# Kernel optimization log

Hardware: AMD Instinct MI355X
Metric: run time of the kernel (lower is better)

The kernel has to match this reference:

```python
import jax, jax.numpy as jnp
import numpy as np

B, N, D = 8, 256, 256
LN_EPS = 1e-5


def setup_inputs() -> dict:
    key = jax.random.key(0)
    ks = jax.random.split(key, 8)
    s1 = 1.0 / np.sqrt(2 * D)  # torch Linear init scale ~ U(-1/sqrt(fan_in), ...); use normal*scale
    s2 = 1.0 / np.sqrt(D)
    return {
        "patch_features": jax.random.normal(ks[0], (B, N, D), dtype=jnp.float32),
        # relation_transform: Linear(2D, D) -> ReLU -> Linear(D, 1)
        "W1": jax.random.normal(ks[1], (2 * D, D), dtype=jnp.float32) * s1,
        "b1": jax.random.normal(ks[2], (D,), dtype=jnp.float32) * s1,
        "W2": jax.random.normal(ks[3], (D, 1), dtype=jnp.float32) * s2,
        "b2": jax.random.normal(ks[4], (1,), dtype=jnp.float32) * s2,
        # context_projection: Linear(D, D) + LayerNorm(D)
        "Wp": jax.random.normal(ks[5], (D, D), dtype=jnp.float32) * s2,
        "bp": jax.random.normal(ks[6], (D,), dtype=jnp.float32) * s2,
        "ln_gamma": jnp.ones((D,), dtype=jnp.float32),
        "ln_beta": jnp.zeros((D,), dtype=jnp.float32),
    }


def reference(patch_features, W1, b1, W2, b2, Wp, bp, ln_gamma, ln_beta):
    x = patch_features  # [B, N, D]
    d = x.shape[-1]
    # cat([x_i, x_j]) @ W1 == x_i @ W1[:D] + x_j @ W1[D:]
    hi = jnp.einsum("bnd,de->bne", x, W1[:d])   # [B, N, D]
    hj = jnp.einsum("bmd,de->bme", x, W1[d:])   # [B, N, D]
    h = jax.nn.relu(hi[:, :, None, :] + hj[:, None, :, :] + b1)  # [B, N, N, D]
    scores = jnp.einsum("bnmd,do->bnm", h, W2) + b2[0]            # [B, N, N]
    # diagonal entries stay exactly 0 (original never fills i == j)
    eye = jnp.eye(scores.shape[1], dtype=bool)
    scores = jnp.where(eye[None, :, :], 0.0, scores)
    weights = jax.nn.softmax(scores, axis=2)                      # [B, N, N]
    ctx = jnp.einsum("bnm,bmd->bnd", weights, x)                  # [B, N, D]
    proj = jnp.einsum("bnd,de->bne", ctx, Wp) + bp
    mu = jnp.mean(proj, axis=-1, keepdims=True)
    var = jnp.mean(jnp.square(proj - mu), axis=-1, keepdims=True)
    ln = (proj - mu) * jax.lax.rsqrt(var + LN_EPS) * ln_gamma + ln_beta
    return x + ln
```

## Files before the change

kernel.cpp:

```cpp
#include <hip/hip_runtime.h>

#define LN_EPS 1e-5f

__device__ __forceinline__ float wred_max(float v) {
#pragma unroll
    for (int off = 32; off; off >>= 1) v = fmaxf(v, __shfl_xor(v, off, 64));
    return v;
}
__device__ __forceinline__ float wred_sum(float v) {
#pragma unroll
    for (int off = 32; off; off >>= 1) v += __shfl_xor(v, off, 64);
    return v;
}


#define GL(Q, KB) { const float* _p = Wb + (size_t)((KB) * 8) * 256;            \
    _Pragma("unroll") for (int _j = 0; _j < 8; _j++)                            \
        Q[_j] = *(const float2*)(_p + (size_t)_j * 256); }

#define GC(Q, KB) { const int _k = (KB) * 8;                                    \
    _Pragma("unroll") for (int _r = 0; _r < 4; _r++) {                          \
        float4 _xa = *(const float4*)(xr + _r * 256 + _k);                      \
        float4 _xb = *(const float4*)(xr + _r * 256 + _k + 4);                  \
        acc[_r][0] = fmaf(_xa.x, Q[0].x, acc[_r][0]);                           \
        acc[_r][1] = fmaf(_xa.x, Q[0].y, acc[_r][1]);                           \
        acc[_r][0] = fmaf(_xa.y, Q[1].x, acc[_r][0]);                           \
        acc[_r][1] = fmaf(_xa.y, Q[1].y, acc[_r][1]);                           \
        acc[_r][0] = fmaf(_xa.z, Q[2].x, acc[_r][0]);                           \
        acc[_r][1] = fmaf(_xa.z, Q[2].y, acc[_r][1]);                           \
        acc[_r][0] = fmaf(_xa.w, Q[3].x, acc[_r][0]);                           \
        acc[_r][1] = fmaf(_xa.w, Q[3].y, acc[_r][1]);                           \
        acc[_r][0] = fmaf(_xb.x, Q[4].x, acc[_r][0]);                           \
        acc[_r][1] = fmaf(_xb.x, Q[4].y, acc[_r][1]);                           \
        acc[_r][0] = fmaf(_xb.y, Q[5].x, acc[_r][0]);                           \
        acc[_r][1] = fmaf(_xb.y, Q[5].y, acc[_r][1]);                           \
        acc[_r][0] = fmaf(_xb.z, Q[6].x, acc[_r][0]);                           \
        acc[_r][1] = fmaf(_xb.z, Q[6].y, acc[_r][1]);                           \
        acc[_r][0] = fmaf(_xb.w, Q[7].x, acc[_r][0]);                           \
        acc[_r][1] = fmaf(_xb.w, Q[7].y, acc[_r][1]); } }

__global__ __launch_bounds__(256) void k_gemm_hij(
    const float* __restrict__ x,
    const float* __restrict__ W1,
    const float* __restrict__ b1,
    float* __restrict__ hi_ws,
    float* __restrict__ hjT)
{
    __shared__ __align__(16) float xs[8][256];
    const int t = threadIdx.x;
    const int lane = t & 63, w = t >> 6;
    const int b = blockIdx.x & 7;
    const int idx = blockIdx.x >> 3;
    const int rg = idx & 31;
    const int half = idx >> 5;
    const int mrow0 = rg * 8;

    {
        const float4* src = (const float4*)(x + (size_t)(b * 256 + mrow0) * 256);
        ((float4*)xs)[t]       = src[t];
        ((float4*)xs)[t + 256] = src[t + 256];
    }
    __syncthreads();

    const int rsub = (w >> 1) * 4;
    const int e0 = ((w & 1) << 7) + 2 * lane;
    const float* Wb = W1 + (size_t)half * 65536 + e0;
    const float* xr = &xs[rsub][0];

    float acc[4][2];
#pragma unroll
    for (int r = 0; r < 4; r++) { acc[r][0] = 0.f; acc[r][1] = 0.f; }

    float2 qa[8], qb[8];
    GL(qa, 0);
    for (int kb = 0; kb + 2 < 32; kb += 2) {
        GL(qb, kb + 1);
        GC(qa, kb);
        GL(qa, kb + 2);
        GC(qb, kb + 1);
    }
    GL(qb, 31);
    GC(qa, 30);
    GC(qb, 31);

    if (half == 0) {
        const int grow0 = b * 256 + mrow0 + rsub;
        float2 bb = *(const float2*)(b1 + e0);
#pragma unroll
        for (int r = 0; r < 4; r++)
            *(float2*)&hi_ws[(size_t)(grow0 + r) * 256 + e0] =
                make_float2(acc[r][0] + bb.x, acc[r][1] + bb.y);
    } else {
        const int m0 = mrow0 + rsub;
        *(float4*)&hjT[(size_t)b * 65536 + (size_t)e0 * 256 + m0] =
            make_float4(acc[0][0], acc[1][0], acc[2][0], acc[3][0]);
        *(float4*)&hjT[(size_t)b * 65536 + (size_t)(e0 + 1) * 256 + m0] =
            make_float4(acc[0][1], acc[1][1], acc[2][1], acc[3][1]);
    }
}


#define P1L(H, G) { const float* _p = hjp + (size_t)((G) * 4) * 256;            \
    _Pragma("unroll") for (int _j = 0; _j < 4; _j++)                            \
        H[_j] = *(const float4*)(_p + (size_t)_j * 256); }

#define P1C(H, G) { const int _db = w * 64 + (G) * 4;                           \
    float4 _wq = *(const float4*)&w2_s[_db];                                    \
    _Pragma("unroll") for (int _n = 0; _n < 4; _n++) {                          \
        float4 _h4 = *(const float4*)&hi_s[_n][_db];                            \
        sp[_n][0] = fmaf(fmaxf(_h4.x + H[0].x, 0.f), _wq.x, sp[_n][0]);         \
        sp[_n][0] = fmaf(fmaxf(_h4.y + H[1].x, 0.f), _wq.y, sp[_n][0]);         \
        sp[_n][0] = fmaf(fmaxf(_h4.z + H[2].x, 0.f), _wq.z, sp[_n][0]);         \
        sp[_n][0] = fmaf(fmaxf(_h4.w + H[3].x, 0.f), _wq.w, sp[_n][0]);         \
        sp[_n][1] = fmaf(fmaxf(_h4.x + H[0].y, 0.f), _wq.x, sp[_n][1]);         \
        sp[_n][1] = fmaf(fmaxf(_h4.y + H[1].y, 0.f), _wq.y, sp[_n][1]);         \
        sp[_n][1] = fmaf(fmaxf(_h4.z + H[2].y, 0.f), _wq.z, sp[_n][1]);         \
        sp[_n][1] = fmaf(fmaxf(_h4.w + H[3].y, 0.f), _wq.w, sp[_n][1]);         \
        sp[_n][2] = fmaf(fmaxf(_h4.x + H[0].z, 0.f), _wq.x, sp[_n][2]);         \
        sp[_n][2] = fmaf(fmaxf(_h4.y + H[1].z, 0.f), _wq.y, sp[_n][2]);         \
        sp[_n][2] = fmaf(fmaxf(_h4.z + H[2].z, 0.f), _wq.z, sp[_n][2]);         \
        sp[_n][2] = fmaf(fmaxf(_h4.w + H[3].z, 0.f), _wq.w, sp[_n][2]);         \
        sp[_n][3] = fmaf(fmaxf(_h4.x + H[0].w, 0.f), _wq.x, sp[_n][3]);         \
        sp[_n][3] = fmaf(fmaxf(_h4.y + H[1].w, 0.f), _wq.y, sp[_n][3]);         \
        sp[_n][3] = fmaf(fmaxf(_h4.z + H[2].w, 0.f), _wq.z, sp[_n][3]);         \
        sp[_n][3] = fmaf(fmaxf(_h4.w + H[3].w, 0.f), _wq.w, sp[_n][3]); } }

#define DLOAD(X, PTR, G) { const float* _p = (PTR) + (size_t)((G) * 8) * 256;   \
    _Pragma("unroll") for (int _j = 0; _j < 8; _j++)                            \
        X[_j] = *(const float4*)(_p + (size_t)_j * 256); }

#define DCOMP(ACCV, WS, X, G) { const int _rb = w * 64 + (G) * 8;               \
    _Pragma("unroll") for (int _n = 0; _n < 4; _n++) {                          \
        float4 _wa = *(const float4*)&WS[_n][_rb];                              \
        float4 _wb = *(const float4*)&WS[_n][_rb + 4];                          \
        ACCV[_n][0] = fmaf(_wa.x, X[0].x, ACCV[_n][0]);                         \
        ACCV[_n][0] = fmaf(_wa.y, X[1].x, ACCV[_n][0]);                         \
        ACCV[_n][0] = fmaf(_wa.z, X[2].x, ACCV[_n][0]);                         \
        ACCV[_n][0] = fmaf(_wa.w, X[3].x, ACCV[_n][0]);                         \
        ACCV[_n][0] = fmaf(_wb.x, X[4].x, ACCV[_n][0]);                         \
        ACCV[_n][0] = fmaf(_wb.y, X[5].x, ACCV[_n][0]);                         \
        ACCV[_n][0] = fmaf(_wb.z, X[6].x, ACCV[_n][0]);                         \
        ACCV[_n][0] = fmaf(_wb.w, X[7].x, ACCV[_n][0]);                         \
        ACCV[_n][1] = fmaf(_wa.x, X[0].y, ACCV[_n][1]);                         \
        ACCV[_n][1] = fmaf(_wa.y, X[1].y, ACCV[_n][1]);                         \
        ACCV[_n][1] = fmaf(_wa.z, X[2].y, ACCV[_n][1]);                         \
        ACCV[_n][1] = fmaf(_wa.w, X[3].y, ACCV[_n][1]);                         \
        ACCV[_n][1] = fmaf(_wb.x, X[4].y, ACCV[_n][1]);                         \
        ACCV[_n][1] = fmaf(_wb.y, X[5].y, ACCV[_n][1]);                         \
        ACCV[_n][1] = fmaf(_wb.z, X[6].y, ACCV[_n][1]);                         \
        ACCV[_n][1] = fmaf(_wb.w, X[7].y, ACCV[_n][1]);                         \
        ACCV[_n][2] = fmaf(_wa.x, X[0].z, ACCV[_n][2]);                         \
        ACCV[_n][2] = fmaf(_wa.y, X[1].z, ACCV[_n][2]);                         \
        ACCV[_n][2] = fmaf(_wa.z, X[2].z, ACCV[_n][2]);                         \
        ACCV[_n][2] = fmaf(_wa.w, X[3].z, ACCV[_n][2]);                         \
        ACCV[_n][2] = fmaf(_wb.x, X[4].z, ACCV[_n][2]);                         \
        ACCV[_n][2] = fmaf(_wb.y, X[5].z, ACCV[_n][2]);                         \
        ACCV[_n][2] = fmaf(_wb.z, X[6].z, ACCV[_n][2]);                         \
        ACCV[_n][2] = fmaf(_wb.w, X[7].z, ACCV[_n][2]);                         \
        ACCV[_n][3] = fmaf(_wa.x, X[0].w, ACCV[_n][3]);                         \
        ACCV[_n][3] = fmaf(_wa.y, X[1].w, ACCV[_n][3]);                         \
        ACCV[_n][3] = fmaf(_wa.z, X[2].w, ACCV[_n][3]);                         \
        ACCV[_n][3] = fmaf(_wa.w, X[3].w, ACCV[_n][3]);                         \
        ACCV[_n][3] = fmaf(_wb.x, X[4].w, ACCV[_n][3]);                         \
        ACCV[_n][3] = fmaf(_wb.y, X[5].w, ACCV[_n][3]);                         \
        ACCV[_n][3] = fmaf(_wb.z, X[6].w, ACCV[_n][3]);                         \
        ACCV[_n][3] = fmaf(_wb.w, X[7].w, ACCV[_n][3]); } }

__global__ __launch_bounds__(256) void k_fused(
    const float* __restrict__ x,
    const float* __restrict__ hi_ws,
    const float* __restrict__ hjT,
    const float* __restrict__ W2, const float* __restrict__ b2,
    const float* __restrict__ Wp, const float* __restrict__ bp,
    const float* __restrict__ gma, const float* __restrict__ bta,
    float* __restrict__ out)
{
    const int t = threadIdx.x;
    const int lane = t & 63, w = t >> 6;
    const int b = blockIdx.x & 7;
    const int n0 = (blockIdx.x >> 3) * 4;
    const int bn0 = b * 256 + n0;

    __shared__ __align__(16) float hi_s[4][256];
    __shared__ __align__(16) float w2_s[256];
    __shared__ __align__(16) float wt_s[4][256];
    __shared__ __align__(16) float ctx_s[4][256];
    __shared__ __align__(16) float sred[4][4][256];
    __shared__ float part[8][4];

#pragma unroll
    for (int i = 0; i < 4; i++) hi_s[i][t] = hi_ws[(size_t)(bn0 + i) * 256 + t];
    w2_s[t] = W2[t];
    __syncthreads();

    {
        const float* hjp = hjT + (size_t)b * 65536 + (size_t)(w * 64) * 256 + 4 * lane;
        float sp[4][4];
#pragma unroll
        for (int n = 0; n < 4; n++)
#pragma unroll
            for (int j = 0; j < 4; j++) sp[n][j] = 0.f;

        float4 ha[4], hb[4];
        P1L(ha, 0);
        for (int g = 0; g + 2 < 16; g += 2) {
            P1L(hb, g + 1);
            P1C(ha, g);
            P1L(ha, g + 2);
            P1C(hb, g + 1);
        }
        P1L(hb, 15);
        P1C(ha, 14);
        P1C(hb, 15);

#pragma unroll
        for (int n = 0; n < 4; n++)
            *(float4*)&sred[w][n][4 * lane] =
                make_float4(sp[n][0], sp[n][1], sp[n][2], sp[n][3]);
    }
    __syncthreads();

    float b2v = b2[0];
    float s[4];
#pragma unroll
    for (int i = 0; i < 4; i++) {
        s[i] = ((sred[0][i][t] + sred[1][i][t]) +
                (sred[2][i][t] + sred[3][i][t])) + b2v;
        if (t == n0 + i) s[i] = 0.f;
    }
#pragma unroll
    for (int i = 0; i < 4; i++) {
        float m = wred_max(s[i]);
        if (lane == 0) part[i][w] = m;
    }
    __syncthreads();
    float ev[4];
#pragma unroll
    for (int i = 0; i < 4; i++) {
        float mx = fmaxf(fmaxf(part[i][0], part[i][1]),
                         fmaxf(part[i][2], part[i][3]));
        ev[i] = __expf(s[i] - mx);
        float sm = wred_sum(ev[i]);
        if (lane == 0) part[4 + i][w] = sm;
    }
    __syncthreads();
#pragma unroll
    for (int i = 0; i < 4; i++) {
        float tot = (part[4 + i][0] + part[4 + i][1]) +
                    (part[4 + i][2] + part[4 + i][3]);
        wt_s[i][t] = ev[i] / tot;
    }
    __syncthreads();

    {
        const float* xpp = x + (size_t)b * 65536 + (size_t)(w * 64) * 256 + 4 * lane;
        float cp[4][4];
#pragma unroll
        for (int n = 0; n < 4; n++)
#pragma unroll
            for (int j = 0; j < 4; j++) cp[n][j] = 0.f;

        float4 xa[8], xb[8];
        DLOAD(xa, xpp, 0);
        for (int g = 0; g + 2 < 8; g += 2) {
            DLOAD(xb, xpp, g + 1);
            DCOMP(cp, wt_s, xa, g);
            DLOAD(xa, xpp, g + 2);
            DCOMP(cp, wt_s, xb, g + 1);
        }
        DLOAD(xb, xpp, 7);
        DCOMP(cp, wt_s, xa, 6);
        DCOMP(cp, wt_s, xb, 7);

#pragma unroll
        for (int n = 0; n < 4; n++)
            *(float4*)&sred[w][n][4 * lane] =
                make_float4(cp[n][0], cp[n][1], cp[n][2], cp[n][3]);
    }
    __syncthreads();
#pragma unroll
    for (int i = 0; i < 4; i++)
        ctx_s[i][t] = (sred[0][i][t] + sred[1][i][t]) +
                      (sred[2][i][t] + sred[3][i][t]);
    __syncthreads();

    {
        const float* wpp = Wp + (size_t)(w * 64) * 256 + 4 * lane;
        float pq[4][4];
#pragma unroll
        for (int n = 0; n < 4; n++)
#pragma unroll
            for (int j = 0; j < 4; j++) pq[n][j] = 0.f;

        float4 qa4[8], qb4[8];
        DLOAD(qa4, wpp, 0);
        for (int g = 0; g + 2 < 8; g += 2) {
            DLOAD(qb4, wpp, g + 1);
            DCOMP(pq, ctx_s, qa4, g);
            DLOAD(qa4, wpp, g + 2);
            DCOMP(pq, ctx_s, qb4, g + 1);
        }
        DLOAD(qb4, wpp, 7);
        DCOMP(pq, ctx_s, qa4, 6);
        DCOMP(pq, ctx_s, qb4, 7);

#pragma unroll
        for (int n = 0; n < 4; n++)
            *(float4*)&sred[w][n][4 * lane] =
                make_float4(pq[n][0], pq[n][1], pq[n][2], pq[n][3]);
    }
    __syncthreads();

    float bpv = bp[t];
    float p[4];
#pragma unroll
    for (int i = 0; i < 4; i++)
        p[i] = ((sred[0][i][t] + sred[1][i][t]) +
                (sred[2][i][t] + sred[3][i][t])) + bpv;

#pragma unroll
    for (int i = 0; i < 4; i++) {
        float su = wred_sum(p[i]);
        float sq = wred_sum(p[i] * p[i]);
        if (lane == 0) { part[i][w] = su; part[4 + i][w] = sq; }
    }
    __syncthreads();
    float gv = gma[t], bv = bta[t];
#pragma unroll
    for (int i = 0; i < 4; i++) {
        float su = (part[i][0] + part[i][1]) + (part[i][2] + part[i][3]);
        float sq = (part[4 + i][0] + part[4 + i][1]) +
                   (part[4 + i][2] + part[4 + i][3]);
        float mu = su * (1.f / 256.f);
        float var = sq * (1.f / 256.f) - mu * mu;
        float ln = (p[i] - mu) * rsqrtf(var + LN_EPS) * gv + bv;
        out[(size_t)(bn0 + i) * 256 + t] = x[(size_t)(bn0 + i) * 256 + t] + ln;
    }
}

extern "C" void kernel_launch(void* const* d_in, const int* in_sizes, int n_in,
                              void* d_out, int out_size, void* d_ws, size_t ws_size,
                              hipStream_t stream) {
    const float* x   = (const float*)d_in[0];
    const float* W1  = (const float*)d_in[1];
    const float* b1  = (const float*)d_in[2];
    const float* W2  = (const float*)d_in[3];
    const float* b2  = (const float*)d_in[4];
    const float* Wp  = (const float*)d_in[5];
    const float* bp  = (const float*)d_in[6];
    const float* gma = (const float*)d_in[7];
    const float* bta = (const float*)d_in[8];
    float* out = (float*)d_out;

    float* hi_ws = (float*)d_ws;
    float* hjT   = hi_ws + (size_t)2048 * 256;

    k_gemm_hij<<<512, 256, 0, stream>>>(x, W1, b1, hi_ws, hjT);
    k_fused<<<512, 256, 0, stream>>>(x, hi_ws, hjT, W2, b2, Wp, bp,
                                     gma, bta, out);
}
```

Measured before the change: 107.8 us.

## Remap hi/hj GEMM threads to one row by eight columns with float4 weight loads

Changes the thread mapping of the first projection GEMM so each thread computes one row and eight output columns, in place of four rows and two columns. Weights are now loaded as float4 rather than float2, and the shared-memory tile is padded to 260 columns to avoid bank conflicts. Launch bounds now request two blocks per SM. In exchange, each weight element is reused across only one row instead of four, which raises global and L2 weight traffic, and the transposed hj stores become scalar strided writes instead of float4.

Result: slower. 121.7 us (+12.9%).

```diff
diff --git a/kernel.cpp b/kernel.cpp
--- a/kernel.cpp
+++ b/kernel.cpp
@@ -14,39 +14,33 @@
 }
 
 
-#define GL(Q, KB) { const float* _p = Wb + (size_t)((KB) * 8) * 256;            \
-    _Pragma("unroll") for (int _j = 0; _j < 8; _j++)                            \
-        Q[_j] = *(const float2*)(_p + (size_t)_j * 256); }
-
-#define GC(Q, KB) { const int _k = (KB) * 8;                                    \
-    _Pragma("unroll") for (int _r = 0; _r < 4; _r++) {                          \
-        float4 _xa = *(const float4*)(xr + _r * 256 + _k);                      \
-        float4 _xb = *(const float4*)(xr + _r * 256 + _k + 4);                  \
-        acc[_r][0] = fmaf(_xa.x, Q[0].x, acc[_r][0]);                           \
-        acc[_r][1] = fmaf(_xa.x, Q[0].y, acc[_r][1]);                           \
-        acc[_r][0] = fmaf(_xa.y, Q[1].x, acc[_r][0]);                           \
-        acc[_r][1] = fmaf(_xa.y, Q[1].y, acc[_r][1]);                           \
-        acc[_r][0] = fmaf(_xa.z, Q[2].x, acc[_r][0]);                           \
-        acc[_r][1] = fmaf(_xa.z, Q[2].y, acc[_r][1]);                           \
-        acc[_r][0] = fmaf(_xa.w, Q[3].x, acc[_r][0]);                           \
-        acc[_r][1] = fmaf(_xa.w, Q[3].y, acc[_r][1]);                           \
-        acc[_r][0] = fmaf(_xb.x, Q[4].x, acc[_r][0]);                           \
-        acc[_r][1] = fmaf(_xb.x, Q[4].y, acc[_r][1]);                           \
-        acc[_r][0] = fmaf(_xb.y, Q[5].x, acc[_r][0]);                           \
-        acc[_r][1] = fmaf(_xb.y, Q[5].y, acc[_r][1]);                           \
-        acc[_r][0] = fmaf(_xb.z, Q[6].x, acc[_r][0]);                           \
-        acc[_r][1] = fmaf(_xb.z, Q[6].y, acc[_r][1]);                           \
-        acc[_r][0] = fmaf(_xb.w, Q[7].x, acc[_r][0]);                           \
-        acc[_r][1] = fmaf(_xb.w, Q[7].y, acc[_r][1]); } }
-
-__global__ __launch_bounds__(256) void k_gemm_hij(
+#define WL(Q, XQ, C) {                                                          \
+    XQ = *(const float4*)&xs[row_local][(C) * 4];                               \
+    const float* _wp = Wb + (size_t)((C) * 4) * 256;                            \
+    _Pragma("unroll") for (int _j = 0; _j < 4; _j++) {                          \
+        Q[2 * _j]     = *(const float4*)(_wp + (size_t)_j * 256);               \
+        Q[2 * _j + 1] = *(const float4*)(_wp + (size_t)_j * 256 + 4); } }
+
+#define WC(Q, XQ) {                                                             \
+    const float _xv[4] = {XQ.x, XQ.y, XQ.z, XQ.w};                              \
+    _Pragma("unroll") for (int _j = 0; _j < 4; _j++) {                          \
+        acc[0] = fmaf(_xv[_j], Q[2 * _j].x, acc[0]);                            \
+        acc[1] = fmaf(_xv[_j], Q[2 * _j].y, acc[1]);                            \
+        acc[2] = fmaf(_xv[_j], Q[2 * _j].z, acc[2]);                            \
+        acc[3] = fmaf(_xv[_j], Q[2 * _j].w, acc[3]);                            \
+        acc[4] = fmaf(_xv[_j], Q[2 * _j + 1].x, acc[4]);                        \
+        acc[5] = fmaf(_xv[_j], Q[2 * _j + 1].y, acc[5]);                        \
+        acc[6] = fmaf(_xv[_j], Q[2 * _j + 1].z, acc[6]);                        \
+        acc[7] = fmaf(_xv[_j], Q[2 * _j + 1].w, acc[7]); } }
+
+__global__ __launch_bounds__(256, 2) void k_gemm_hij(
     const float* __restrict__ x,
     const float* __restrict__ W1,
     const float* __restrict__ b1,
     float* __restrict__ hi_ws,
     float* __restrict__ hjT)
 {
-    __shared__ __align__(16) float xs[8][256];
+    __shared__ __align__(16) float xs[8][260];
     const int t = threadIdx.x;
     const int lane = t & 63, w = t >> 6;
     const int b = blockIdx.x & 7;
@@ -56,46 +50,48 @@
     const int mrow0 = rg * 8;
 
     {
-        const float4* src = (const float4*)(x + (size_t)(b * 256 + mrow0) * 256);
-        ((float4*)xs)[t]       = src[t];
-        ((float4*)xs)[t + 256] = src[t + 256];
-    }
-    __syncthreads();
-
-    const int rsub = (w >> 1) * 4;
-    const int e0 = ((w & 1) << 7) + 2 * lane;
-    const float* Wb = W1 + (size_t)half * 65536 + e0;
-    const float* xr = &xs[rsub][0];
-
-    float acc[4][2];
-#pragma unroll
-    for (int r = 0; r < 4; r++) { acc[r][0] = 0.f; acc[r][1] = 0.f; }
-
-    float2 qa[8], qb[8];
-    GL(qa, 0);
-    for (int kb = 0; kb + 2 < 32; kb += 2) {
-        GL(qb, kb + 1);
-        GC(qa, kb);
-        GL(qa, kb + 2);
-        GC(qb, kb + 1);
-    }
-    GL(qb, 31);
-    GC(qa, 30);
-    GC(qb, 31);
+        const int sr = t >> 5;
+        const int sc = (t & 31) * 8;
+        const float* sp = x + (size_t)(b * 256 + mrow0 + sr) * 256 + sc;
+        *(float4*)&xs[sr][sc]     = *(const float4*)sp;
+        *(float4*)&xs[sr][sc + 4] = *(const float4*)(sp + 4);
+    }
+    __syncthreads();
+
+    const int row_local = lane & 7;
+    const int c0 = w * 64 + (lane >> 3) * 8;
+    const float* Wb = W1 + (size_t)half * 65536 + c0;
+
+    float acc[8];
+#pragma unroll
+    for (int j = 0; j < 8; j++) acc[j] = 0.f;
+
+    float4 qa[8], qb[8];
+    float4 xa, xb;
+    WL(qa, xa, 0);
+    for (int c = 0; c + 2 < 64; c += 2) {
+        WL(qb, xb, c + 1);
+        WC(qa, xa);
+        WL(qa, xa, c + 2);
+        WC(qb, xb);
+    }
+    WL(qb, xb, 63);
+    WC(qa, xa);
+    WC(qb, xb);
 
     if (half == 0) {
-        const int grow0 = b * 256 + mrow0 + rsub;
-        float2 bb = *(const float2*)(b1 + e0);
-#pragma unroll
-        for (int r = 0; r < 4; r++)
-            *(float2*)&hi_ws[(size_t)(grow0 + r) * 256 + e0] =
-                make_float2(acc[r][0] + bb.x, acc[r][1] + bb.y);
+        const float4 bb0 = *(const float4*)(b1 + c0);
+        const float4 bb1 = *(const float4*)(b1 + c0 + 4);
+        float* dst = hi_ws + (size_t)(b * 256 + mrow0 + row_local) * 256 + c0;
+        *(float4*)dst = make_float4(acc[0] + bb0.x, acc[1] + bb0.y,
+                                    acc[2] + bb0.z, acc[3] + bb0.w);
+        *(float4*)(dst + 4) = make_float4(acc[4] + bb1.x, acc[5] + bb1.y,
+                                          acc[6] + bb1.z, acc[7] + bb1.w);
     } else {
-        const int m0 = mrow0 + rsub;
-        *(float4*)&hjT[(size_t)b * 65536 + (size_t)e0 * 256 + m0] =
-            make_float4(acc[0][0], acc[1][0], acc[2][0], acc[3][0]);
-        *(float4*)&hjT[(size_t)b * 65536 + (size_t)(e0 + 1) * 256 + m0] =
-            make_float4(acc[0][1], acc[1][1], acc[2][1], acc[3][1]);
+        const int m = mrow0 + row_local;
+        float* base = hjT + (size_t)b * 65536 + (size_t)c0 * 256 + m;
+#pragma unroll
+        for (int j = 0; j < 8; j++) base[(size_t)j * 256] = acc[j];
     }
 }
 
```
